# Kernel optimization log

Hardware: AMD Instinct MI355X
Metric: run time of the kernel (lower is better)

Reference implementation:

```python
import jax, jax.numpy as jnp
import numpy as np

B, H, M, R, DH = 4, 16, 2048, 32, 64
ROPE_BASE = 10000.0
NEG = -1e30  # finite stand-in for -inf masking


def setup_inputs() -> dict:
    key = jax.random.key(0)
    ks = jax.random.split(key, 9)
    s = 0.1
    inp = {
        'Pq': jax.random.normal(ks[0], (B, H, M, R), jnp.float32) * s,
        'Pk': jax.random.normal(ks[1], (B, H, M, R), jnp.float32) * s,
        'Pv': jax.random.normal(ks[2], (B, H, M, R), jnp.float32) * s,
        'Vq': jax.random.normal(ks[3], (H, R, DH), jnp.float32) * s,
        'Vk': jax.random.normal(ks[4], (H, R, DH), jnp.float32) * s,
        'Vv': jax.random.normal(ks[5], (H, R, DH), jnp.float32) * s,
        'bq': jax.random.normal(ks[6], (H * DH,), jnp.float32) * s,
        'bk': jax.random.normal(ks[7], (H * DH,), jnp.float32) * s,
        'bv': jax.random.normal(ks[8], (H * DH,), jnp.float32) * s,
        'attention_mask': jnp.ones((B, M), jnp.int32),
        'position_ids': jnp.broadcast_to(jnp.arange(M, dtype=jnp.int32)[None, :], (B, M)),
    }
    return inp


def _rope_half(x, c, s):
    # kernel semantics: split dh into halves, rotate with SAME cos/sin for both halves
    h = x.shape[-1] // 2
    x0, x1 = x[..., :h], x[..., h:]
    return jnp.concatenate([x0 * c - x1 * s, x0 * s + x1 * c], axis=-1)


def reference(Pq, Pk, Pv, Vq, Vk, Vv, bq, bk, bv, attention_mask, position_ids):
    Bs, Hs, Ms, Rs = Pq.shape
    dh = Vq.shape[-1]
    # --- cos/sin exactly as _build_cos_sin_bmd: interleaved duplication, kernel reads first dh/2 ---
    inv_freq = 1.0 / (ROPE_BASE ** (jnp.arange(0, dh, 2, dtype=jnp.float32) / dh))  # [dh/2]
    ang = position_ids.astype(jnp.float32)[..., None] * inv_freq  # [B,M,dh/2]
    ang_i = jnp.repeat(ang, 2, axis=-1)[..., : dh // 2]  # [c0,c0,c1,c1,...] first half
    cos = jnp.cos(ang_i)[:, None]  # [B,1,M,dh/2]
    sin = jnp.sin(ang_i)[:, None]
    # --- low-rank reconstruction of Q/K/V (+ flat per-head biases) ---
    Q = jnp.einsum('bhmr,hrd->bhmd', Pq, Vq) + bq.reshape(Hs, 1, dh)
    K = jnp.einsum('bhmr,hrd->bhmd', Pk, Vk) + bk.reshape(Hs, 1, dh)
    V = jnp.einsum('bhmr,hrd->bhmd', Pv, Vv) + bv.reshape(Hs, 1, dh)
    # --- inline RoPE ---
    Qr = _rope_half(Q, cos, sin)
    Kr = _rope_half(K, cos, sin)
    # --- attention: causal + pad mask, stable softmax ---
    scale = 1.0 / jnp.sqrt(jnp.float32(dh))
    scores = jnp.einsum('bhmd,bhnd->bhmn', Qr, Kr) * scale
    causal = jnp.tril(jnp.ones((Ms, Ms), dtype=bool))
    mask = causal[None, None, :, :] & (attention_mask > 0)[:, None, None, :]
    scores = jnp.where(mask, scores, NEG)
    p = jax.nn.softmax(scores, axis=-1)
    # kernel zeroes fully-masked rows (l_i == 0)
    any_valid = mask.any(axis=-1, keepdims=True)
    p = jnp.where(any_valid, p, 0.0)
    O = jnp.einsum('bhmn,bhnd->bhmd', p, V)
    return O.transpose(0, 2, 1, 3)  # [B,M,H,dh]
```

## Files before the change

### kernel.cpp

```cpp
#include <hip/hip_runtime.h>
#include <math.h>


#define B_ 4
#define H_ 16
#define M_ 2048
#define R_ 32
#define DH_ 64
#define BH_ 64
#define NEGV -1.0e30f
#define LOG2E 1.4426950408889634f

typedef float  f32x4  __attribute__((ext_vector_type(4)));
typedef __bf16 bf16x8 __attribute__((ext_vector_type(8)));
typedef unsigned short ushort8 __attribute__((ext_vector_type(8)));

__device__ __forceinline__ unsigned short bfbits(float f) {
    __bf16 h = (__bf16)f;
    return __builtin_bit_cast(unsigned short, h);
}

__global__ void prep_kernel(const int* __restrict__ pid,
                            const float* __restrict__ Vq,
                            const float* __restrict__ Vk,
                            const float* __restrict__ Vv,
                            float* __restrict__ tab,
                            unsigned short* __restrict__ VTb)
{
    const int idx = blockIdx.x * 256 + threadIdx.x;
    if (idx < B_ * M_ * 16) {
        const int bm = idx >> 4, fi = idx & 15;
        const float invf = powf(10000.0f, -(float)fi * (1.0f / 32.0f));
        const float ang  = (float)pid[bm] * invf;
        float s, c;
        sincosf(ang, &s, &c);
        tab[(size_t)bm * 32 + fi]      = c;
        tab[(size_t)bm * 32 + 16 + fi] = s;
    } else {
        const int k = idx - B_ * M_ * 16;
        const float* src = (k < 32768) ? Vq : ((k < 65536) ? Vk : Vv);
        const int rem = k & 32767;
        const int h = rem >> 11, d = (rem >> 5) & 63, r = rem & 31;
        VTb[k] = bfbits(src[(h * 32 + r) * 64 + d]);
    }
}

__global__ __launch_bounds__(256) void qkv_proj_mfma_kernel(
    const float* __restrict__ Pq, const float* __restrict__ Pk,
    const float* __restrict__ Pv,
    const unsigned short* __restrict__ VTb,
    const float* __restrict__ bq, const float* __restrict__ bk,
    const float* __restrict__ bv,
    const float* __restrict__ tab,
    unsigned short* __restrict__ Qb, unsigned short* __restrict__ Kb,
    unsigned short* __restrict__ Vt)
{
    const int mat = blockIdx.z, bh = blockIdx.y, m0 = blockIdx.x * 128;
    const int h = bh & (H_ - 1), b = bh >> 4;
    const int t = threadIdx.x, w = t >> 6, lane = t & 63;
    const int c16 = lane & 15, g = lane >> 4, g8 = g << 3;

    const float* P    = (mat == 0) ? Pq : ((mat == 1) ? Pk : Pv);
    const float* bias = (mat == 0) ? bq : ((mat == 1) ? bk : bv);
    const float scl = (mat == 0) ? 0.125f * LOG2E : 1.0f;

    bf16x8 vf[4];
    #pragma unroll
    for (int di = 0; di < 4; ++di)
        vf[di] = *(const bf16x8*)&VTb[((size_t)((mat * 16 + h) * 64 + di * 16 + c16)) * 32 + g8];

    bf16x8 af[2];
    #pragma unroll
    for (int mi = 0; mi < 2; ++mi) {
        const float* p = P + ((size_t)bh * M_ + m0 + w * 32 + mi * 16 + c16) * 32 + g8;
        const f32x4 lo = *(const f32x4*)p;
        const f32x4 hi = *(const f32x4*)(p + 4);
        #pragma unroll
        for (int e = 0; e < 4; ++e) { af[mi][e] = (__bf16)lo[e]; af[mi][4 + e] = (__bf16)hi[e]; }
    }

    f32x4 acc[2][4];
    const f32x4 z4 = {0.f, 0.f, 0.f, 0.f};
    #pragma unroll
    for (int mi = 0; mi < 2; ++mi)
        #pragma unroll
        for (int di = 0; di < 4; ++di)
            acc[mi][di] = __builtin_amdgcn_mfma_f32_16x16x32_bf16(af[mi], vf[di], z4, 0, 0, 0);

    float bsv[4];
    #pragma unroll
    for (int di = 0; di < 4; ++di) bsv[di] = bias[h * 64 + di * 16 + c16];

    if (mat == 2) {
        #pragma unroll
        for (int di = 0; di < 4; ++di) {
            ushort8 v8;
            #pragma unroll
            for (int mi = 0; mi < 2; ++mi)
                #pragma unroll
                for (int reg = 0; reg < 4; ++reg)
                    v8[(mi << 2) | reg] = bfbits(acc[mi][di][reg] + bsv[di]);
            const int d = di * 16 + c16;
            *(ushort8*)&Vt[((size_t)(bh * 64 + d)) * M_ + m0 + w * 32 + g8] = v8;
        }
    } else {
        unsigned short* Out = (mat == 0) ? Qb : Kb;
        #pragma unroll
        for (int mi = 0; mi < 2; ++mi)
            #pragma unroll
            for (int reg = 0; reg < 4; ++reg) {
                const int m = m0 + w * 32 + mi * 16 + (g << 2) + reg;
                const float x0 = acc[mi][0][reg] + bsv[0];
                const float x1 = acc[mi][1][reg] + bsv[1];
                const float x2 = acc[mi][2][reg] + bsv[2];
                const float x3 = acc[mi][3][reg] + bsv[3];
                const size_t o = ((size_t)bh * M_ + m) * 64;
                const size_t bm = (size_t)b * M_ + m;
                const int fi = c16 >> 1;
                const float c0 = tab[bm * 32 + fi],     s0 = tab[bm * 32 + 16 + fi];
                const float c1 = tab[bm * 32 + 8 + fi], s1 = tab[bm * 32 + 24 + fi];
                Out[o + c16]      = bfbits((x0 * c0 - x2 * s0) * scl);
                Out[o + 16 + c16] = bfbits((x1 * c1 - x3 * s1) * scl);
                Out[o + 32 + c16] = bfbits((x0 * s0 + x2 * c0) * scl);
                Out[o + 48 + c16] = bfbits((x1 * s1 + x3 * c1) * scl);
            }
    }
}

__global__ __launch_bounds__(256, 3) void flash_mfma_kernel(
    const unsigned short* __restrict__ Qus, const unsigned short* __restrict__ Kus,
    const unsigned short* __restrict__ Vtus, const int* __restrict__ amask,
    float* __restrict__ out)
{
    __shared__ unsigned short Ks[64 * 72];
    __shared__ unsigned short Vts[64 * 72];
    __shared__ int ams[64];

    const int bh = blockIdx.y;
    const int h  = bh & (H_ - 1), b = bh >> 4;
    const int t  = threadIdx.x;
    const int w  = t >> 6, lane = t & 63;
    const int c16 = lane & 15, g = lane >> 4;
    const int g4 = g << 2, g8 = g << 3;
    const int w32 = w << 5;
    const int srow = t >> 2, sc0 = (t & 3) << 4;

    const unsigned short* Kg  = Kus  + (size_t)bh * M_ * 64;
    const unsigned short* Vtg = Vtus + (size_t)bh * 64 * M_;
    const f32x4 zero4 = {0.f, 0.f, 0.f, 0.f};

    bf16x8 onesf;
    #pragma unroll
    for (int e = 0; e < 8; ++e) onesf[e] = (__bf16)1.0f;

    for (int pick = 0; pick < 2; ++pick) {
        const int qt = pick ? blockIdx.x : (15 - blockIdx.x);
        const int q0 = qt << 7;
        const int nkt = 2 * qt + 2;

        bf16x8 qf[2][2];
        #pragma unroll
        for (int qi = 0; qi < 2; ++qi)
            #pragma unroll
            for (int kkd = 0; kkd < 2; ++kkd)
                qf[qi][kkd] = *(const bf16x8*)(Qus +
                    ((size_t)bh * M_ + q0 + w32 + qi * 16 + c16) * 64 + kkd * 32 + g8);
        const int qrow0 = q0 + w32 + c16;
        const int qrow1 = qrow0 + 16;

        f32x4 oT[4][2];
        #pragma unroll
        for (int di = 0; di < 4; ++di) { oT[di][0] = zero4; oT[di][1] = zero4; }
        f32x4 lacc[2] = {zero4, zero4};
        float mr[2] = {-3.0e38f, -3.0e38f};

        ushort8 kreg0, kreg1, vreg0, vreg1;
        int amreg = 0;
        {
            const unsigned short* gk = Kg + (size_t)srow * 64 + sc0;
            kreg0 = *(const ushort8*)gk; kreg1 = *(const ushort8*)(gk + 8);
            const unsigned short* gv = Vtg + (size_t)srow * M_ + sc0;
            vreg0 = *(const ushort8*)gv; vreg1 = *(const ushort8*)(gv + 8);
            if (t < 64) amreg = amask[b * M_ + t];
        }

        for (int kt = 0; kt < nkt; ++kt) {
            const int n0 = kt << 6;
            __syncthreads();
            *(ushort8*)&Ks[srow * 72 + sc0]      = kreg0;
            *(ushort8*)&Ks[srow * 72 + sc0 + 8]  = kreg1;
            *(ushort8*)&Vts[srow * 72 + sc0]     = vreg0;
            *(ushort8*)&Vts[srow * 72 + sc0 + 8] = vreg1;
            if (t < 64) ams[t] = amreg;
            __syncthreads();

            if (kt + 1 < nkt) {
                const int n1 = n0 + 64;
                const unsigned short* gk = Kg + (size_t)(n1 + srow) * 64 + sc0;
                kreg0 = *(const ushort8*)gk; kreg1 = *(const ushort8*)(gk + 8);
                const unsigned short* gv = Vtg + (size_t)srow * M_ + n1 + sc0;
                vreg0 = *(const ushort8*)gv; vreg1 = *(const ushort8*)(gv + 8);
                if (t < 64) amreg = amask[b * M_ + n1 + t];
            }

            f32x4 st[4][2];
            #pragma unroll
            for (int ni = 0; ni < 4; ++ni) { st[ni][0] = zero4; st[ni][1] = zero4; }
            __builtin_amdgcn_s_setprio(1);
            #pragma unroll
            for (int kkd = 0; kkd < 2; ++kkd)
                #pragma unroll
                for (int ni = 0; ni < 4; ++ni) {
                    const bf16x8 kf = *(const bf16x8*)&Ks[(ni * 16 + c16) * 72 + kkd * 32 + g8];
                    st[ni][0] = __builtin_amdgcn_mfma_f32_16x16x32_bf16(kf, qf[0][kkd], st[ni][0], 0, 0, 0);
                    st[ni][1] = __builtin_amdgcn_mfma_f32_16x16x32_bf16(kf, qf[1][kkd], st[ni][1], 0, 0, 0);
                }
            __builtin_amdgcn_s_setprio(0);

            const bool allv  = __all(ams[lane] > 0);
            const bool needc = (n0 + 63) > (q0 + w32);
            bf16x8 pf[2][2];
            #pragma unroll
            for (int qi = 0; qi < 2; ++qi) {
                const int qrow = qi ? qrow1 : qrow0;
                float tm = -3.0e38f;
                if (allv) {
                    if (needc) {
                        #pragma unroll
                        for (int ni = 0; ni < 4; ++ni)
                            #pragma unroll
                            for (int rg = 0; rg < 4; ++rg) {
                                const int n_loc = ni * 16 + g4 + rg;
                                const float sv = ((n0 + n_loc) <= qrow) ? st[ni][qi][rg] : NEGV;
                                st[ni][qi][rg] = sv;
                                tm = fmaxf(tm, sv);
                            }
                    } else {
                        #pragma unroll
                        for (int ni = 0; ni < 4; ++ni)
                            #pragma unroll
                            for (int rg = 0; rg < 4; ++rg)
                                tm = fmaxf(tm, st[ni][qi][rg]);
                    }
                } else {
                    #pragma unroll
                    for (int ni = 0; ni < 4; ++ni)
                        #pragma unroll
                        for (int rg = 0; rg < 4; ++rg) {
                            const int n_loc = ni * 16 + g4 + rg;
                            const bool ok = ((n0 + n_loc) <= qrow) && (ams[n_loc] > 0);
                            const float sv = ok ? st[ni][qi][rg] : NEGV;
                            st[ni][qi][rg] = sv;
                            tm = fmaxf(tm, sv);
                        }
                }
                tm = fmaxf(tm, __shfl_xor(tm, 16));
                tm = fmaxf(tm, __shfl_xor(tm, 32));
                const bool skip = __all(tm <= mr[qi] + 7.0f);
                if (!skip) {
                    const float mnew  = fmaxf(mr[qi], tm);
                    const float alpha = exp2f(mr[qi] - mnew);
                    mr[qi] = mnew;
                    #pragma unroll
                    for (int di = 0; di < 4; ++di)
                        #pragma unroll
                        for (int rg = 0; rg < 4; ++rg)
                            oT[di][qi][rg] *= alpha;
                    lacc[qi][0] *= alpha;
                }
                const float mcur = mr[qi];
                if (allv) {
                    #pragma unroll
                    for (int ni = 0; ni < 4; ++ni)
                        #pragma unroll
                        for (int rg = 0; rg < 4; ++rg)
                            pf[ni >> 1][qi][((ni & 1) << 2) | rg] =
                                (__bf16)exp2f(st[ni][qi][rg] - mcur);
                } else {
                    #pragma unroll
                    for (int ni = 0; ni < 4; ++ni)
                        #pragma unroll
                        for (int rg = 0; rg < 4; ++rg) {
                            const float sv = st[ni][qi][rg];
                            const float pv = (sv > -1.0e29f) ? exp2f(sv - mcur) : 0.f;
                            pf[ni >> 1][qi][((ni & 1) << 2) | rg] = (__bf16)pv;
                        }
                }
            }

            __builtin_amdgcn_s_setprio(1);
            lacc[0] = __builtin_amdgcn_mfma_f32_16x16x32_bf16(onesf, pf[0][0], lacc[0], 0, 0, 0);
            lacc[0] = __builtin_amdgcn_mfma_f32_16x16x32_bf16(onesf, pf[1][0], lacc[0], 0, 0, 0);
            lacc[1] = __builtin_amdgcn_mfma_f32_16x16x32_bf16(onesf, pf[0][1], lacc[1], 0, 0, 0);
            lacc[1] = __builtin_amdgcn_mfma_f32_16x16x32_bf16(onesf, pf[1][1], lacc[1], 0, 0, 0);
            #pragma unroll
            for (int di = 0; di < 4; ++di)
                #pragma unroll
                for (int kk = 0; kk < 2; ++kk) {
                    const bf16x8 vfr = *(const bf16x8*)&Vts[(di * 16 + c16) * 72 + kk * 32 + g8];
                    oT[di][0] = __builtin_amdgcn_mfma_f32_16x16x32_bf16(vfr, pf[kk][0], oT[di][0], 0, 0, 0);
                    oT[di][1] = __builtin_amdgcn_mfma_f32_16x16x32_bf16(vfr, pf[kk][1], oT[di][1], 0, 0, 0);
                }
            __builtin_amdgcn_s_setprio(0);
        }

        float inv[2];
        inv[0] = (lacc[0][0] > 0.f) ? 1.f / lacc[0][0] : 0.f;
        inv[1] = (lacc[1][0] > 0.f) ? 1.f / lacc[1][0] : 0.f;
        #pragma unroll
        for (int di = 0; di < 4; ++di)
            #pragma unroll
            for (int qi = 0; qi < 2; ++qi) {
                const int q = q0 + w32 + qi * 16 + c16;
                f32x4 ov;
                #pragma unroll
                for (int rg = 0; rg < 4; ++rg) ov[rg] = oT[di][qi][rg] * inv[qi];
                *(f32x4*)&out[((size_t)(b * M_ + q) * H_ + h) * 64 + di * 16 + g4] = ov;
            }
    }
}

extern "C" void kernel_launch(void* const* d_in, const int* in_sizes, int n_in,
                              void* d_out, int out_size, void* d_ws, size_t ws_size,
                              hipStream_t stream)
{
    const float* Pq = (const float*)d_in[0];
    const float* Pk = (const float*)d_in[1];
    const float* Pv = (const float*)d_in[2];
    const float* Vq = (const float*)d_in[3];
    const float* Vk = (const float*)d_in[4];
    const float* Vv = (const float*)d_in[5];
    const float* bq = (const float*)d_in[6];
    const float* bk = (const float*)d_in[7];
    const float* bv = (const float*)d_in[8];
    const int*   am = (const int*)d_in[9];
    const int*   pid = (const int*)d_in[10];
    float* out = (float*)d_out;

    float* tab = (float*)d_ws;
    unsigned short* VTb = (unsigned short*)((char*)d_ws + (1 << 20));
    unsigned short* Qb  = (unsigned short*)((char*)d_ws + (2 << 20));
    unsigned short* Kb = Qb + (size_t)B_ * H_ * M_ * 64;
    unsigned short* Vt = Kb + (size_t)B_ * H_ * M_ * 64;

    prep_kernel<<<dim3((B_ * M_ * 16 + 98304) / 256), dim3(256), 0, stream>>>(
        pid, Vq, Vk, Vv, tab, VTb);

    qkv_proj_mfma_kernel<<<dim3(16, 64, 3), dim3(256), 0, stream>>>(
        Pq, Pk, Pv, VTb, bq, bk, bv, tab, Qb, Kb, Vt);

    flash_mfma_kernel<<<dim3(8, BH_), dim3(256), 0, stream>>>(
        Qb, Kb, Vt, am, out);
}
```

Baseline: 211.2 us.

## Shrink flash query tile to 64 rows, remap blocks per XCD, stage P via LDS

Measured after the change: 200.2 us. 1.05x faster.

```diff
diff --git a/kernel.cpp b/kernel.cpp
--- a/kernel.cpp
+++ b/kernel.cpp
@@ -13,7 +13,8 @@
 
 typedef float  f32x4  __attribute__((ext_vector_type(4)));
 typedef __bf16 bf16x8 __attribute__((ext_vector_type(8)));
-typedef unsigned short ushort8 __attribute__((ext_vector_type(8)));
+typedef unsigned short u16x4 __attribute__((ext_vector_type(4)));
+typedef unsigned short u16x8 __attribute__((ext_vector_type(8)));
 
 __device__ __forceinline__ unsigned short bfbits(float f) {
     __bf16 h = (__bf16)f;
@@ -55,6 +56,8 @@
     unsigned short* __restrict__ Qb, unsigned short* __restrict__ Kb,
     unsigned short* __restrict__ Vt)
 {
+    __shared__ unsigned short Ps[128 * 40];
+
     const int mat = blockIdx.z, bh = blockIdx.y, m0 = blockIdx.x * 128;
     const int h = bh & (H_ - 1), b = bh >> 4;
     const int t = threadIdx.x, w = t >> 6, lane = t & 63;
@@ -64,20 +67,29 @@
     const float* bias = (mat == 0) ? bq : ((mat == 1) ? bk : bv);
     const float scl = (mat == 0) ? 0.125f * LOG2E : 1.0f;
 
+    const float* Pg = P + ((size_t)bh * M_ + m0) * 32;
+    #pragma unroll
+    for (int pass = 0; pass < 4; ++pass) {
+        const int lin = pass * 256 + t;
+        const int row = lin >> 3, c4 = (lin & 7) << 2;
+        const f32x4 v = *(const f32x4*)&Pg[row * 32 + c4];
+        u16x4 b4;
+        #pragma unroll
+        for (int e = 0; e < 4; ++e) b4[e] = bfbits(v[e]);
+        *(u16x4*)&Ps[row * 40 + c4] = b4;
+    }
+
     bf16x8 vf[4];
     #pragma unroll
     for (int di = 0; di < 4; ++di)
         vf[di] = *(const bf16x8*)&VTb[((size_t)((mat * 16 + h) * 64 + di * 16 + c16)) * 32 + g8];
 
+    __syncthreads();
+
     bf16x8 af[2];
     #pragma unroll
-    for (int mi = 0; mi < 2; ++mi) {
-        const float* p = P + ((size_t)bh * M_ + m0 + w * 32 + mi * 16 + c16) * 32 + g8;
-        const f32x4 lo = *(const f32x4*)p;
-        const f32x4 hi = *(const f32x4*)(p + 4);
-        #pragma unroll
-        for (int e = 0; e < 4; ++e) { af[mi][e] = (__bf16)lo[e]; af[mi][4 + e] = (__bf16)hi[e]; }
-    }
+    for (int mi = 0; mi < 2; ++mi)
+        af[mi] = *(const bf16x8*)&Ps[(w * 32 + mi * 16 + c16) * 40 + g8];
 
     f32x4 acc[2][4];
     const f32x4 z4 = {0.f, 0.f, 0.f, 0.f};
@@ -94,14 +106,14 @@
     if (mat == 2) {
         #pragma unroll
         for (int di = 0; di < 4; ++di) {
-            ushort8 v8;
+            u16x8 v8;
             #pragma unroll
             for (int mi = 0; mi < 2; ++mi)
                 #pragma unroll
                 for (int reg = 0; reg < 4; ++reg)
                     v8[(mi << 2) | reg] = bfbits(acc[mi][di][reg] + bsv[di]);
             const int d = di * 16 + c16;
-            *(ushort8*)&Vt[((size_t)(bh * 64 + d)) * M_ + m0 + w * 32 + g8] = v8;
+            *(u16x8*)&Vt[((size_t)(bh * 64 + d)) * M_ + m0 + w * 32 + g8] = v8;
         }
     } else {
         unsigned short* Out = (mat == 0) ? Qb : Kb;
@@ -127,7 +139,7 @@
     }
 }
 
-__global__ __launch_bounds__(256, 3) void flash_mfma_kernel(
+__global__ __launch_bounds__(256, 4) void flash_mfma_kernel(
     const unsigned short* __restrict__ Qus, const unsigned short* __restrict__ Kus,
     const unsigned short* __restrict__ Vtus, const int* __restrict__ amask,
     float* __restrict__ out)
@@ -136,13 +148,16 @@
     __shared__ unsigned short Vts[64 * 72];
     __shared__ int ams[64];
 
-    const int bh = blockIdx.y;
-    const int h  = bh & (H_ - 1), b = bh >> 4;
-    const int t  = threadIdx.x;
-    const int w  = t >> 6, lane = t & 63;
+    const int bid = blockIdx.x;
+    const int xcd = bid & 7, loc = bid >> 3;
+    const int bh  = xcd * 8 + (loc & 7);
+    const int px  = loc >> 3;
+    const int h = bh & (H_ - 1), b = bh >> 4;
+    const int t = threadIdx.x;
+    const int w = t >> 6, lane = t & 63;
     const int c16 = lane & 15, g = lane >> 4;
     const int g4 = g << 2, g8 = g << 3;
-    const int w32 = w << 5;
+    const int w16 = w << 4;
     const int srow = t >> 2, sc0 = (t & 3) << 4;
 
     const unsigned short* Kg  = Kus  + (size_t)bh * M_ * 64;
@@ -154,75 +169,69 @@
     for (int e = 0; e < 8; ++e) onesf[e] = (__bf16)1.0f;
 
     for (int pick = 0; pick < 2; ++pick) {
-        const int qt = pick ? blockIdx.x : (15 - blockIdx.x);
-        const int q0 = qt << 7;
-        const int nkt = 2 * qt + 2;
-
-        bf16x8 qf[2][2];
-        #pragma unroll
-        for (int qi = 0; qi < 2; ++qi)
-            #pragma unroll
-            for (int kkd = 0; kkd < 2; ++kkd)
-                qf[qi][kkd] = *(const bf16x8*)(Qus +
-                    ((size_t)bh * M_ + q0 + w32 + qi * 16 + c16) * 64 + kkd * 32 + g8);
-        const int qrow0 = q0 + w32 + c16;
-        const int qrow1 = qrow0 + 16;
-
-        f32x4 oT[4][2];
-        #pragma unroll
-        for (int di = 0; di < 4; ++di) { oT[di][0] = zero4; oT[di][1] = zero4; }
-        f32x4 lacc[2] = {zero4, zero4};
-        float mr[2] = {-3.0e38f, -3.0e38f};
-
-        ushort8 kreg0, kreg1, vreg0, vreg1;
+        const int qt = pick ? px : (31 - px);
+        const int q0 = qt << 6;
+        const int nkt = qt + 1;
+
+        bf16x8 qf[2];
+        #pragma unroll
+        for (int kkd = 0; kkd < 2; ++kkd)
+            qf[kkd] = *(const bf16x8*)(Qus +
+                ((size_t)bh * M_ + q0 + w16 + c16) * 64 + kkd * 32 + g8);
+        const int qrow = q0 + w16 + c16;
+
+        f32x4 oT[4];
+        #pragma unroll
+        for (int di = 0; di < 4; ++di) oT[di] = zero4;
+        f32x4 lacc = zero4;
+        float mr = -3.0e38f;
+
+        u16x8 kreg0, kreg1, vreg0, vreg1;
         int amreg = 0;
         {
             const unsigned short* gk = Kg + (size_t)srow * 64 + sc0;
-            kreg0 = *(const ushort8*)gk; kreg1 = *(const ushort8*)(gk + 8);
+            kreg0 = *(const u16x8*)gk; kreg1 = *(const u16x8*)(gk + 8);
             const unsigned short* gv = Vtg + (size_t)srow * M_ + sc0;
-            vreg0 = *(const ushort8*)gv; vreg1 = *(const ushort8*)(gv + 8);
+            vreg0 = *(const u16x8*)gv; vreg1 = *(const u16x8*)(gv + 8);
             if (t < 64) amreg = amask[b * M_ + t];
         }
 
         for (int kt = 0; kt < nkt; ++kt) {
             const int n0 = kt << 6;
             __syncthreads();
-            *(ushort8*)&Ks[srow * 72 + sc0]      = kreg0;
-            *(ushort8*)&Ks[srow * 72 + sc0 + 8]  = kreg1;
-            *(ushort8*)&Vts[srow * 72 + sc0]     = vreg0;
-            *(ushort8*)&Vts[srow * 72 + sc0 + 8] = vreg1;
+            *(u16x8*)&Ks[srow * 72 + sc0]      = kreg0;
+            *(u16x8*)&Ks[srow * 72 + sc0 + 8]  = kreg1;
+            *(u16x8*)&Vts[srow * 72 + sc0]     = vreg0;
+            *(u16x8*)&Vts[srow * 72 + sc0 + 8] = vreg1;
             if (t < 64) ams[t] = amreg;
             __syncthreads();
 
             if (kt + 1 < nkt) {
                 const int n1 = n0 + 64;
                 const unsigned short* gk = Kg + (size_t)(n1 + srow) * 64 + sc0;
-                kreg0 = *(const ushort8*)gk; kreg1 = *(const ushort8*)(gk + 8);
+                kreg0 = *(const u16x8*)gk; kreg1 = *(const u16x8*)(gk + 8);
                 const unsigned short* gv = Vtg + (size_t)srow * M_ + n1 + sc0;
-                vreg0 = *(const ushort8*)gv; vreg1 = *(const ushort8*)(gv + 8);
+                vreg0 = *(const u16x8*)gv; vreg1 = *(const u16x8*)(gv + 8);
                 if (t < 64) amreg = amask[b * M_ + n1 + t];
             }
 
-            f32x4 st[4][2];
-            #pragma unroll
-            for (int ni = 0; ni < 4; ++ni) { st[ni][0] = zero4; st[ni][1] = zero4; }
+            f32x4 st[4];
+            #pragma unroll
+            for (int ni = 0; ni < 4; ++ni) st[ni] = zero4;
             __builtin_amdgcn_s_setprio(1);
             #pragma unroll
             for (int kkd = 0; kkd < 2; ++kkd)
                 #pragma unroll
                 for (int ni = 0; ni < 4; ++ni) {
                     const bf16x8 kf = *(const bf16x8*)&Ks[(ni * 16 + c16) * 72 + kkd * 32 + g8];
-                    st[ni][0] = __builtin_amdgcn_mfma_f32_16x16x32_bf16(kf, qf[0][kkd], st[ni][0], 0, 0, 0);
-                    st[ni][1] = __builtin_amdgcn_mfma_f32_16x16x32_bf16(kf, qf[1][kkd], st[ni][1], 0, 0, 0);
+                    st[ni] = __builtin_amdgcn_mfma_f32_16x16x32_bf16(kf, qf[kkd], st[ni], 0, 0, 0);
                 }
             __builtin_amdgcn_s_setprio(0);
 
             const bool allv  = __all(ams[lane] > 0);
-            const bool needc = (n0 + 63) > (q0 + w32);
-            bf16x8 pf[2][2];
-            #pragma unroll
-            for (int qi = 0; qi < 2; ++qi) {
-                const int qrow = qi ? qrow1 : qrow0;
+            const bool needc = (n0 + 63) > (q0 + w16);
+            bf16x8 pf[2];
+            {
                 float tm = -3.0e38f;
                 if (allv) {
                     if (needc) {
@@ -231,8 +240,8 @@
                             #pragma unroll
                             for (int rg = 0; rg < 4; ++rg) {
                                 const int n_loc = ni * 16 + g4 + rg;
-                                const float sv = ((n0 + n_loc) <= qrow) ? st[ni][qi][rg] : NEGV;
-                                st[ni][qi][rg] = sv;
+                                const float sv = ((n0 + n_loc) <= qrow) ? st[ni][rg] : NEGV;
+                                st[ni][rg] = sv;
                                 tm = fmaxf(tm, sv);
                             }
                     } else {
@@ -240,7 +249,7 @@
                         for (int ni = 0; ni < 4; ++ni)
                             #pragma unroll
                             for (int rg = 0; rg < 4; ++rg)
-                                tm = fmaxf(tm, st[ni][qi][rg]);
+                                tm = fmaxf(tm, st[ni][rg]);
                     }
                 } else {
                     #pragma unroll
@@ -249,74 +258,66 @@
                         for (int rg = 0; rg < 4; ++rg) {
                             const int n_loc = ni * 16 + g4 + rg;
                             const bool ok = ((n0 + n_loc) <= qrow) && (ams[n_loc] > 0);
-                            const float sv = ok ? st[ni][qi][rg] : NEGV;
-                            st[ni][qi][rg] = sv;
+                            const float sv = ok ? st[ni][rg] : NEGV;
+                            st[ni][rg] = sv;
                             tm = fmaxf(tm, sv);
                         }
                 }
                 tm = fmaxf(tm, __shfl_xor(tm, 16));
                 tm = fmaxf(tm, __shfl_xor(tm, 32));
-                const bool skip = __all(tm <= mr[qi] + 7.0f);
+                const bool skip = __all(tm <= mr + 7.0f);
                 if (!skip) {
-                    const float mnew  = fmaxf(mr[qi], tm);
-                    const float alpha = exp2f(mr[qi] - mnew);
-                    mr[qi] = mnew;
+                    const float mnew  = fmaxf(mr, tm);
+                    const float alpha = exp2f(mr - mnew);
+                    mr = mnew;
                     #pragma unroll
                     for (int di = 0; di < 4; ++di)
                         #pragma unroll
                         for (int rg = 0; rg < 4; ++rg)
-                            oT[di][qi][rg] *= alpha;
-                    lacc[qi][0] *= alpha;
-                }
-                const float mcur = mr[qi];
+                            oT[di][rg] *= alpha;
+                    lacc[0] *= alpha;
+                }
                 if (allv) {
                     #pragma unroll
                     for (int ni = 0; ni < 4; ++ni)
                         #pragma unroll
                         for (int rg = 0; rg < 4; ++rg)
-                            pf[ni >> 1][qi][((ni & 1) << 2) | rg] =
-                                (__bf16)exp2f(st[ni][qi][rg] - mcur);
+                            pf[ni >> 1][((ni & 1) << 2) | rg] =
+                                (__bf16)exp2f(st[ni][rg] - mr);
                 } else {
                     #pragma unroll
                     for (int ni = 0; ni < 4; ++ni)
                         #pragma unroll
                         for (int rg = 0; rg < 4; ++rg) {
-                            const float sv = st[ni][qi][rg];
-                            const float pv = (sv > -1.0e29f) ? exp2f(sv - mcur) : 0.f;
-                            pf[ni >> 1][qi][((ni & 1) << 2) | rg] = (__bf16)pv;
+                            const float sv = st[ni][rg];
+                            const float pv = (sv > -1.0e29f) ? exp2f(sv - mr) : 0.f;
+                            pf[ni >> 1][((ni & 1) << 2) | rg] = (__bf16)pv;
                         }
                 }
             }
 
             __builtin_amdgcn_s_setprio(1);
-            lacc[0] = __builtin_amdgcn_mfma_f32_16x16x32_bf16(onesf, pf[0][0], lacc[0], 0, 0, 0);
-            lacc[0] = __builtin_amdgcn_mfma_f32_16x16x32_bf16(onesf, pf[1][0], lacc[0], 0, 0, 0);
-            lacc[1] = __builtin_amdgcn_mfma_f32_16x16x32_bf16(onesf, pf[0][1], lacc[1], 0, 0, 0);
-            lacc[1] = __builtin_amdgcn_mfma_f32_16x16x32_bf16(onesf, pf[1][1], lacc[1], 0, 0, 0);
+            lacc = __builtin_amdgcn_mfma_f32_16x16x32_bf16(onesf, pf[0], lacc, 0, 0, 0);
+            lacc = __builtin_amdgcn_mfma_f32_16x16x32_bf16(onesf, pf[1], lacc, 0, 0, 0);
             #pragma unroll
             for (int di = 0; di < 4; ++di)
                 #pragma unroll
                 for (int kk = 0; kk < 2; ++kk) {
                     const bf16x8 vfr = *(const bf16x8*)&Vts[(di * 16 + c16) * 72 + kk * 32 + g8];
-                    oT[di][0] = __builtin_amdgcn_mfma_f32_16x16x32_bf16(vfr, pf[kk][0], oT[di][0], 0, 0, 0);
-                    oT[di][1] = __builtin_amdgcn_mfma_f32_16x16x32_bf16(vfr, pf[kk][1], oT[di][1], 0, 0, 0);
+                    oT[di] = __builtin_amdgcn_mfma_f32_16x16x32_bf16(vfr, pf[kk], oT[di], 0, 0, 0);
                 }
             __builtin_amdgcn_s_setprio(0);
         }
 
-        float inv[2];
-        inv[0] = (lacc[0][0] > 0.f) ? 1.f / lacc[0][0] : 0.f;
-        inv[1] = (lacc[1][0] > 0.f) ? 1.f / lacc[1][0] : 0.f;
-        #pragma unroll
-        for (int di = 0; di < 4; ++di)
-            #pragma unroll
-            for (int qi = 0; qi < 2; ++qi) {
-                const int q = q0 + w32 + qi * 16 + c16;
-                f32x4 ov;
-                #pragma unroll
-                for (int rg = 0; rg < 4; ++rg) ov[rg] = oT[di][qi][rg] * inv[qi];
-                *(f32x4*)&out[((size_t)(b * M_ + q) * H_ + h) * 64 + di * 16 + g4] = ov;
-            }
+        const float inv = (lacc[0] > 0.f) ? 1.f / lacc[0] : 0.f;
+        const int q = q0 + w16 + c16;
+        #pragma unroll
+        for (int di = 0; di < 4; ++di) {
+            f32x4 ov;
+            #pragma unroll
+            for (int rg = 0; rg < 4; ++rg) ov[rg] = oT[di][rg] * inv;
+            *(f32x4*)&out[((size_t)(b * M_ + q) * H_ + h) * 64 + di * 16 + g4] = ov;
+        }
     }
 }
 
@@ -349,6 +350,6 @@
     qkv_proj_mfma_kernel<<<dim3(16, 64, 3), dim3(256), 0, stream>>>(
         Pq, Pk, Pv, VTb, bq, bk, bv, tab, Qb, Kb, Vt);
 
-    flash_mfma_kernel<<<dim3(8, BH_), dim3(256), 0, stream>>>(
+    flash_mfma_kernel<<<dim3(1024), dim3(256), 0, stream>>>(
         Qb, Kb, Vt, am, out);
 }
```
